# Optimization experiments

Measured on AMD Instinct MI355X. Metric: run time of the kernel, lower is better.

Reference implementation:

```python
import jax, jax.numpy as jnp
import numpy as np

# module hyperparameters (from init_kwargs)
STRIDE, PAD, DIL = 1, 1, 1
GROUPS, DG = 1, 1
KH, KW = 3, 3
CIN, COUT = 256, 256


def _mdcn_forward(x, offset, mask, weight, bias):
    B, C, H, W = x.shape
    Cout = weight.shape[0]
    K = KH * KW
    Ho = (H + 2 * PAD - (DIL * (KH - 1) + 1)) // STRIDE + 1
    Wo = (W + 2 * PAD - (DIL * (KW - 1) + 1)) // STRIDE + 1
    Cg = C // DG

    # offset channel layout: ((g*K + k)*2 + {0: dy, 1: dx})
    off = offset.reshape(B, DG, KH, KW, 2, Ho, Wo)
    base_y = (jnp.arange(Ho) * STRIDE - PAD)[None, :] + DIL * jnp.arange(KH)[:, None]  # [KH,Ho]
    base_x = (jnp.arange(Wo) * STRIDE - PAD)[None, :] + DIL * jnp.arange(KW)[:, None]  # [KW,Wo]
    sy = base_y[None, None, :, None, :, None].astype(x.dtype) + off[:, :, :, :, 0]  # [B,DG,KH,KW,Ho,Wo]
    sx = base_x[None, None, None, :, None, :].astype(x.dtype) + off[:, :, :, :, 1]

    y0f = jnp.floor(sy); x0f = jnp.floor(sx)
    wy = sy - y0f; wx = sx - x0f
    y0 = y0f.astype(jnp.int32); x0 = x0f.astype(jnp.int32)

    xg = x.reshape(B, DG, Cg, H * W)

    def corner(yc, xc, w):
        valid = (yc >= 0) & (yc < H) & (xc >= 0) & (xc < W)
        idx = jnp.clip(yc, 0, H - 1) * W + jnp.clip(xc, 0, W - 1)  # [B,DG,KH,KW,Ho,Wo]
        v = jnp.take_along_axis(xg, idx.reshape(B, DG, 1, -1), axis=3)  # [B,DG,Cg,K*Ho*Wo]
        v = v.reshape(B, DG, Cg, KH, KW, Ho, Wo)
        return v * (w * valid.astype(x.dtype))[:, :, None]

    val = (corner(y0, x0, (1 - wy) * (1 - wx))
           + corner(y0, x0 + 1, (1 - wy) * wx)
           + corner(y0 + 1, x0, wy * (1 - wx))
           + corner(y0 + 1, x0 + 1, wy * wx))  # [B,DG,Cg,KH,KW,Ho,Wo]

    cols = val * mask.reshape(B, DG, 1, KH, KW, Ho, Wo)
    cols = cols.reshape(B, GROUPS, (C // GROUPS) * K, Ho * Wo)
    wg = weight.reshape(GROUPS, Cout // GROUPS, (C // GROUPS) * K)
    out = jnp.einsum('gok,bgkp->bgop', wg, cols).reshape(B, Cout, Ho, Wo)
    return out + bias[None, :, None, None]


def setup_inputs() -> dict:
    key = jax.random.key(0)
    k1, k2, k3, k4 = jax.random.split(key, 4)
    B, H, W = 4, 64, 64
    x = jax.random.normal(k1, (B, CIN, H, W), dtype=jnp.float32)
    offset = jax.random.normal(k2, (B, 2 * DG * KH * KW, H, W), dtype=jnp.float32)
    mask = jax.random.uniform(k3, (B, DG * KH * KW, H, W), dtype=jnp.float32)
    stdv = 1.0 / np.sqrt(CIN * KH * KW)
    weight = jax.random.uniform(k4, (COUT, CIN // GROUPS, KH, KW), dtype=jnp.float32,
                                minval=-stdv, maxval=stdv)
    bias = jnp.zeros((COUT,), dtype=jnp.float32)
    return {"x": x, "offset": offset, "mask": mask, "weight": weight, "bias": bias}


def reference(x, offset, mask, weight, bias):
    return _mdcn_forward(x, offset, mask, weight, bias)
```

## Files before the change

### kernel.cpp

```cpp
#include <hip/hip_runtime.h>
#include <hip/hip_bf16.h>
#include <stdint.h>

#define KDIM 2304

typedef __bf16 bf16_t;
typedef bf16_t bf16x8 __attribute__((ext_vector_type(8)));
typedef float f32x4 __attribute__((ext_vector_type(4)));
typedef float f32x2 __attribute__((ext_vector_type(2)));

__device__ __forceinline__ float b2f_lo(uint32_t u) {
  union { uint32_t i; float f; } c; c.i = u << 16; return c.f;
}
__device__ __forceinline__ float b2f_hi(uint32_t u) {
  union { uint32_t i; float f; } c; c.i = u & 0xffff0000u; return c.f;
}
__device__ __forceinline__ uint32_t pk_bf16(float a, float b) {
  __hip_bfloat162 h = __float22bfloat162_rn(make_float2(a, b));
  union { __hip_bfloat162 h; uint32_t u; } c; c.h = h; return c.u;
}

__device__ __forceinline__ uint4 blend8(const uint4 d[4], const float cw[4]) {
  f32x2 f0 = {0.f, 0.f}, f1 = {0.f, 0.f}, f2 = {0.f, 0.f}, f3 = {0.f, 0.f};
#pragma unroll
  for (int c = 0; c < 4; ++c) {
    f32x2 wc = {cw[c], cw[c]};
    f0 += wc * f32x2{b2f_lo(d[c].x), b2f_hi(d[c].x)};
    f1 += wc * f32x2{b2f_lo(d[c].y), b2f_hi(d[c].y)};
    f2 += wc * f32x2{b2f_lo(d[c].z), b2f_hi(d[c].z)};
    f3 += wc * f32x2{b2f_lo(d[c].w), b2f_hi(d[c].w)};
  }
  uint4 o;
  o.x = pk_bf16(f0.x, f0.y);
  o.y = pk_bf16(f1.x, f1.y);
  o.z = pk_bf16(f2.x, f2.y);
  o.w = pk_bf16(f3.x, f3.y);
  return o;
}

__global__ __launch_bounds__(256) void k_prep(const float* __restrict__ x,
                                              uint16_t* __restrict__ xt,
                                              const float* __restrict__ w,
                                              uint16_t* __restrict__ wt2) {
  int tid = threadIdx.x;
  if (blockIdx.x < 1024) {
    __shared__ float tile[64][65];
    int b = blockIdx.x >> 8;
    int cgrp = (blockIdx.x >> 6) & 3;
    int sgrp = blockIdx.x & 63;
    int c0 = cgrp << 6, s0 = sgrp << 6;
#pragma unroll
    for (int it = 0; it < 4; ++it) {
      int f = tid + it * 256;
      int rr = f >> 4, col = (f & 15) << 2;
      float4 v = *(const float4*)&x[((size_t)(b * 256 + c0 + rr)) * 4096 + s0 + col];
      tile[rr][col + 0] = v.x;
      tile[rr][col + 1] = v.y;
      tile[rr][col + 2] = v.z;
      tile[rr][col + 3] = v.w;
    }
    __syncthreads();
    int sp = tid >> 2, cb = (tid & 3) * 16;
    uint4 o1, o2;
    o1.x = pk_bf16(tile[cb + 0][sp], tile[cb + 1][sp]);
    o1.y = pk_bf16(tile[cb + 2][sp], tile[cb + 3][sp]);
    o1.z = pk_bf16(tile[cb + 4][sp], tile[cb + 5][sp]);
    o1.w = pk_bf16(tile[cb + 6][sp], tile[cb + 7][sp]);
    o2.x = pk_bf16(tile[cb + 8][sp], tile[cb + 9][sp]);
    o2.y = pk_bf16(tile[cb + 10][sp], tile[cb + 11][sp]);
    o2.z = pk_bf16(tile[cb + 12][sp], tile[cb + 13][sp]);
    o2.w = pk_bf16(tile[cb + 14][sp], tile[cb + 15][sp]);
    uint16_t* dst = &xt[((size_t)(b * 4096 + s0 + sp)) * 256 + c0 + cb];
    *(uint4*)dst = o1;
    *(uint4*)(dst + 8) = o2;
  } else {
    __shared__ float wl[2304];
    int row = blockIdx.x - 1024;
    const float* wrow = w + (size_t)row * KDIM;
    for (int i2 = tid; i2 < 2304; i2 += 256) wl[i2] = wrow[i2];
    __syncthreads();
    int strip = row >> 4, r16 = row & 15;
    for (int c = tid; c < 288; c += 256) {
      int tap = c >> 5, rem = c & 31;
      int w64 = rem >> 3, kh = (rem >> 2) & 1, seg = rem & 3;
      int i = tap * 4 + w64;
      int cin0 = w64 * 64 + kh * 32 + seg * 8;
      int lanex = seg * 16 + r16;
      uint16_t* dst = wt2 + (size_t)i * 16384 + (size_t)(strip * 128 + kh * 64 + lanex) * 8;
      uint4 o;
      o.x = pk_bf16(wl[(cin0 + 0) * 9 + tap], wl[(cin0 + 1) * 9 + tap]);
      o.y = pk_bf16(wl[(cin0 + 2) * 9 + tap], wl[(cin0 + 3) * 9 + tap]);
      o.z = pk_bf16(wl[(cin0 + 4) * 9 + tap], wl[(cin0 + 5) * 9 + tap]);
      o.w = pk_bf16(wl[(cin0 + 6) * 9 + tap], wl[(cin0 + 7) * 9 + tap]);
      *(uint4*)dst = o;
    }
  }
}

__device__ __forceinline__ void mk_corners(int tap, int p, int ho,
                                           const float* s_off, const float* s_msk,
                                           float cw[4], int cpo[4]) {
  int kh = tap / 3, kw = tap - kh * 3;
  float dy = s_off[(2 * tap) * 64 + p];
  float dx = s_off[(2 * tap + 1) * 64 + p];
  float mm = s_msk[tap * 64 + p];
  float sy = (float)(ho - 1 + kh) + dy;
  float sx = (float)(p - 1 + kw) + dx;
  float fy = floorf(sy), fx = floorf(sx);
  int y0 = (int)fy, x0 = (int)fx;
  float wy = sy - fy, wx = sx - fx;
#pragma unroll
  for (int cy = 0; cy < 2; ++cy) {
#pragma unroll
    for (int cx = 0; cx < 2; ++cx) {
      int y = y0 + cy, xx = x0 + cx;
      float wgt = (cy ? wy : 1.f - wy) * (cx ? wx : 1.f - wx) * mm;
      bool v = ((unsigned)y < 64u) && ((unsigned)xx < 64u);
      wgt = v ? wgt : 0.f;
      int yc = min(max(y, 0), 63), xc = min(max(xx, 0), 63);
      cw[cy * 2 + cx] = wgt;
      cpo[cy * 2 + cx] = ((yc << 6) + xc) * 256;
    }
  }
}

__global__ __launch_bounds__(1024, 4) void k_fused(const uint16_t* __restrict__ xt,
                                                   const uint16_t* __restrict__ wt2,
                                                   const float* __restrict__ off,
                                                   const float* __restrict__ msk,
                                                   const float* __restrict__ bias,
                                                   float* __restrict__ out) {
  constexpr int ROWU = 272;
  constexpr int BUFU = 64 * ROWU;
  __shared__ __align__(16) uint16_t Bs[2 * BUFU];
  __shared__ float s_off[18 * 64];
  __shared__ float s_msk[9 * 64];

  int tid = threadIdx.x;
  int swz = ((int)blockIdx.x & 7) * 32 + ((int)blockIdx.x >> 3);
  int b = swz >> 6, ho = swz & 63;

  const float* offb = off + (size_t)b * 18 * 4096 + ho * 64;
  for (int i = tid; i < 18 * 64; i += 1024)
    s_off[i] = offb[(size_t)(i >> 6) * 4096 + (i & 63)];
  const float* mskb = msk + (size_t)b * 9 * 4096 + ho * 64;
  for (int i = tid; i < 9 * 64; i += 1024)
    s_msk[i] = mskb[(size_t)(i >> 6) * 4096 + (i & 63)];

  int lane = tid & 63, wv = tid >> 6;
  int wm = wv >> 1, wn = wv & 1;
  int q = lane >> 4, r = lane & 15;
  int p = tid >> 4, cg16 = tid & 15;
  int sA = cg16 >> 3, cg = cg16 & 7;
  const uint16_t* xtb = xt + (size_t)b * 1048576 + cg * 8;
  int chwA = sA * 64, chwB = chwA + 128;
  int ch = cg ^ (p & 7);
  int wcolA = p * ROWU + sA * 64 + ch * 8;
  int wcolB = wcolA + 128;

  f32x4 acc[2][2];
#pragma unroll
  for (int mi = 0; mi < 2; ++mi)
#pragma unroll
    for (int ni = 0; ni < 2; ++ni) acc[mi][ni] = f32x4{0.f, 0.f, 0.f, 0.f};

  __syncthreads();

  float cw[4];
  int cpo[4];
  uint4 dnvA[4], dnvB[4];

  int c0 = (q ^ (r & 7)) << 3;
  int c1 = c0 ^ 32;
  int rowb0 = (wn * 32 + r) * ROWU;

  mk_corners(0, p, ho, s_off, s_msk, cw, cpo);
#pragma unroll
  for (int c = 0; c < 4; ++c) dnvA[c] = *(const uint4*)(xtb + cpo[c] + chwA);
#pragma unroll
  for (int c = 0; c < 4; ++c) dnvB[c] = *(const uint4*)(xtb + cpo[c] + chwB);
  *(uint4*)(Bs + wcolA) = blend8(dnvA, cw);
  *(uint4*)(Bs + wcolB) = blend8(dnvB, cw);
  __syncthreads();

#define PHASE(S)                                                                \
    {                                                                           \
      const uint16_t* wp = wpb + (S) * 16384;                                   \
      bf16x8 a00 = *(const bf16x8*)(wp);                           \
      bf16x8 a01 = *(const bf16x8*)(wp + 512);                     \
      bf16x8 a10 = *(const bf16x8*)(wp + 1024);                    \
      bf16x8 a11 = *(const bf16x8*)(wp + 1536);                    \
      const uint16_t* br = bsrow + rowb0 + (S) * 64;                            \
      bf16x8 b0k0 = *(const bf16x8*)(br + c0);                                  \
      bf16x8 b0k1 = *(const bf16x8*)(br + c1);                                  \
      bf16x8 b1k0 = *(const bf16x8*)(br + 16 * ROWU + c0);                      \
      bf16x8 b1k1 = *(const bf16x8*)(br + 16 * ROWU + c1);                      \
      __builtin_amdgcn_s_setprio(1);                                            \
      acc[0][0] = __builtin_amdgcn_mfma_f32_16x16x32_bf16(a00, b0k0, acc[0][0], 0, 0, 0); \
      acc[0][1] = __builtin_amdgcn_mfma_f32_16x16x32_bf16(a00, b1k0, acc[0][1], 0, 0, 0); \
      acc[1][0] = __builtin_amdgcn_mfma_f32_16x16x32_bf16(a10, b0k0, acc[1][0], 0, 0, 0); \
      acc[1][1] = __builtin_amdgcn_mfma_f32_16x16x32_bf16(a10, b1k0, acc[1][1], 0, 0, 0); \
      acc[0][0] = __builtin_amdgcn_mfma_f32_16x16x32_bf16(a01, b0k1, acc[0][0], 0, 0, 0); \
      acc[0][1] = __builtin_amdgcn_mfma_f32_16x16x32_bf16(a01, b1k1, acc[0][1], 0, 0, 0); \
      acc[1][0] = __builtin_amdgcn_mfma_f32_16x16x32_bf16(a11, b0k1, acc[1][0], 0, 0, 0); \
      acc[1][1] = __builtin_amdgcn_mfma_f32_16x16x32_bf16(a11, b1k1, acc[1][1], 0, 0, 0); \
      __builtin_amdgcn_s_setprio(0);                                            \
    }

#pragma unroll 1
  for (int i = 0; i < 9; ++i) {
    if (i < 8) {
      mk_corners(i + 1, p, ho, s_off, s_msk, cw, cpo);
#pragma unroll
      for (int c = 0; c < 4; ++c) dnvA[c] = *(const uint4*)(xtb + cpo[c] + chwA);
#pragma unroll
      for (int c = 0; c < 4; ++c) dnvB[c] = *(const uint4*)(xtb + cpo[c] + chwB);
    }
    const uint16_t* wpb = wt2 + (size_t)(4 * i) * 16384 + wm * 2048 + lane * 8;
    const uint16_t* bsrow = Bs + (i & 1) * BUFU;
    PHASE(0)
    __builtin_amdgcn_sched_barrier(0);
    PHASE(1)
    __builtin_amdgcn_sched_barrier(0);
    PHASE(2)
    __builtin_amdgcn_sched_barrier(0);
    PHASE(3)
    if (i < 8) {
      uint16_t* wdst = Bs + ((i + 1) & 1) * BUFU;
      *(uint4*)(wdst + wcolA) = blend8(dnvA, cw);
      *(uint4*)(wdst + wcolB) = blend8(dnvB, cw);
    }
    __syncthreads();
  }
#undef PHASE

#pragma unroll
  for (int mi = 0; mi < 2; ++mi) {
#pragma unroll
    for (int j = 0; j < 4; ++j) {
      int m = wm * 32 + mi * 16 + q * 4 + j;
      float bv = bias[m];
#pragma unroll
      for (int ni = 0; ni < 2; ++ni) {
        int wog = wn * 32 + ni * 16 + r;
        out[((size_t)(b * 256 + m)) * 4096 + ho * 64 + wog] = acc[mi][ni][j] + bv;
      }
    }
  }
}

extern "C" void kernel_launch(void* const* d_in, const int* in_sizes, int n_in,
                              void* d_out, int out_size, void* d_ws, size_t ws_size,
                              hipStream_t stream) {
  (void)in_sizes; (void)n_in; (void)out_size; (void)ws_size;
  const float* x      = (const float*)d_in[0];
  const float* offset = (const float*)d_in[1];
  const float* mask   = (const float*)d_in[2];
  const float* weight = (const float*)d_in[3];
  const float* bias   = (const float*)d_in[4];
  float* out = (float*)d_out;

  uint8_t* ws = (uint8_t*)d_ws;
  uint16_t* xt  = (uint16_t*)ws;
  uint16_t* wt2 = (uint16_t*)(ws + 8388608);

  k_prep<<<dim3(1280), 256, 0, stream>>>(x, xt, weight, wt2);
  k_fused<<<dim3(256), 1024, 0, stream>>>(xt, wt2, offset, mask, bias, out);
}
```

Before: 119.0 us.

## Software-pipeline MFMA operand loads and interleave gather/blend across phases

Restructures the K-loop so the weight (A) and LDS (B) fragments for the next phase are loaded into a second register set while the current phase's MFMAs run. The offset-corner gathers and bilinear blends for the next tap are spread across the phases instead of being issued all at once up front. This hides global and LDS latency behind matrix math. The cost is more live vector registers, which may lower occupancy or cause spills.

```diff
diff --git a/kernel.cpp b/kernel.cpp
--- a/kernel.cpp
+++ b/kernel.cpp
@@ -169,70 +169,92 @@
   float cw[4];
   int cpo[4];
   uint4 dnvA[4], dnvB[4];
+  uint4 oA, oB;
+  bf16x8 X00, X01, X10, X11, Y00, Y01, Y10, Y11;
+  bf16x8 U0k0, U0k1, U1k0, U1k1, V0k0, V0k1, V1k0, V1k1;
 
   int c0 = (q ^ (r & 7)) << 3;
   int c1 = c0 ^ 32;
   int rowb0 = (wn * 32 + r) * ROWU;
 
+#define LOAD_A(P, BASE)                                                         \
+  P##00 = *(const bf16x8*)(BASE);                                               \
+  P##01 = *(const bf16x8*)((BASE) + 512);                                       \
+  P##10 = *(const bf16x8*)((BASE) + 1024);                                      \
+  P##11 = *(const bf16x8*)((BASE) + 1536);
+#define LOAD_B(P, OFS)                                                          \
+  P##0k0 = *(const bf16x8*)(bsrow + rowb0 + (OFS) + c0);                        \
+  P##0k1 = *(const bf16x8*)(bsrow + rowb0 + (OFS) + c1);                        \
+  P##1k0 = *(const bf16x8*)(bsrow + rowb0 + 16 * ROWU + (OFS) + c0);            \
+  P##1k1 = *(const bf16x8*)(bsrow + rowb0 + 16 * ROWU + (OFS) + c1);
+#define MFMA8(A, B)                                                             \
+  __builtin_amdgcn_s_setprio(1);                                                \
+  acc[0][0] = __builtin_amdgcn_mfma_f32_16x16x32_bf16(A##00, B##0k0, acc[0][0], 0, 0, 0); \
+  acc[0][1] = __builtin_amdgcn_mfma_f32_16x16x32_bf16(A##00, B##1k0, acc[0][1], 0, 0, 0); \
+  acc[1][0] = __builtin_amdgcn_mfma_f32_16x16x32_bf16(A##10, B##0k0, acc[1][0], 0, 0, 0); \
+  acc[1][1] = __builtin_amdgcn_mfma_f32_16x16x32_bf16(A##10, B##1k0, acc[1][1], 0, 0, 0); \
+  acc[0][0] = __builtin_amdgcn_mfma_f32_16x16x32_bf16(A##01, B##0k1, acc[0][0], 0, 0, 0); \
+  acc[0][1] = __builtin_amdgcn_mfma_f32_16x16x32_bf16(A##01, B##1k1, acc[0][1], 0, 0, 0); \
+  acc[1][0] = __builtin_amdgcn_mfma_f32_16x16x32_bf16(A##11, B##0k1, acc[1][0], 0, 0, 0); \
+  acc[1][1] = __builtin_amdgcn_mfma_f32_16x16x32_bf16(A##11, B##1k1, acc[1][1], 0, 0, 0); \
+  __builtin_amdgcn_s_setprio(0);
+
   mk_corners(0, p, ho, s_off, s_msk, cw, cpo);
 #pragma unroll
   for (int c = 0; c < 4; ++c) dnvA[c] = *(const uint4*)(xtb + cpo[c] + chwA);
 #pragma unroll
   for (int c = 0; c < 4; ++c) dnvB[c] = *(const uint4*)(xtb + cpo[c] + chwB);
+  {
+    const uint16_t* wp0 = wt2 + wm * 2048 + lane * 8;
+    LOAD_A(X, wp0)
+  }
   *(uint4*)(Bs + wcolA) = blend8(dnvA, cw);
   *(uint4*)(Bs + wcolB) = blend8(dnvB, cw);
   __syncthreads();
 
-#define PHASE(S)                                                                \
-    {                                                                           \
-      const uint16_t* wp = wpb + (S) * 16384;                                   \
-      bf16x8 a00 = *(const bf16x8*)(wp);                           \
-      bf16x8 a01 = *(const bf16x8*)(wp + 512);                     \
-      bf16x8 a10 = *(const bf16x8*)(wp + 1024);                    \
-      bf16x8 a11 = *(const bf16x8*)(wp + 1536);                    \
-      const uint16_t* br = bsrow + rowb0 + (S) * 64;                            \
-      bf16x8 b0k0 = *(const bf16x8*)(br + c0);                                  \
-      bf16x8 b0k1 = *(const bf16x8*)(br + c1);                                  \
-      bf16x8 b1k0 = *(const bf16x8*)(br + 16 * ROWU + c0);                      \
-      bf16x8 b1k1 = *(const bf16x8*)(br + 16 * ROWU + c1);                      \
-      __builtin_amdgcn_s_setprio(1);                                            \
-      acc[0][0] = __builtin_amdgcn_mfma_f32_16x16x32_bf16(a00, b0k0, acc[0][0], 0, 0, 0); \
-      acc[0][1] = __builtin_amdgcn_mfma_f32_16x16x32_bf16(a00, b1k0, acc[0][1], 0, 0, 0); \
-      acc[1][0] = __builtin_amdgcn_mfma_f32_16x16x32_bf16(a10, b0k0, acc[1][0], 0, 0, 0); \
-      acc[1][1] = __builtin_amdgcn_mfma_f32_16x16x32_bf16(a10, b1k0, acc[1][1], 0, 0, 0); \
-      acc[0][0] = __builtin_amdgcn_mfma_f32_16x16x32_bf16(a01, b0k1, acc[0][0], 0, 0, 0); \
-      acc[0][1] = __builtin_amdgcn_mfma_f32_16x16x32_bf16(a01, b1k1, acc[0][1], 0, 0, 0); \
-      acc[1][0] = __builtin_amdgcn_mfma_f32_16x16x32_bf16(a11, b0k1, acc[1][0], 0, 0, 0); \
-      acc[1][1] = __builtin_amdgcn_mfma_f32_16x16x32_bf16(a11, b1k1, acc[1][1], 0, 0, 0); \
-      __builtin_amdgcn_s_setprio(0);                                            \
-    }
-
 #pragma unroll 1
   for (int i = 0; i < 9; ++i) {
-    if (i < 8) {
-      mk_corners(i + 1, p, ho, s_off, s_msk, cw, cpo);
-#pragma unroll
-      for (int c = 0; c < 4; ++c) dnvA[c] = *(const uint4*)(xtb + cpo[c] + chwA);
-#pragma unroll
-      for (int c = 0; c < 4; ++c) dnvB[c] = *(const uint4*)(xtb + cpo[c] + chwB);
-    }
     const uint16_t* wpb = wt2 + (size_t)(4 * i) * 16384 + wm * 2048 + lane * 8;
     const uint16_t* bsrow = Bs + (i & 1) * BUFU;
-    PHASE(0)
+    bool more = (i < 8);
+    LOAD_B(U, 0)
+    if (more) {
+      mk_corners(i + 1, p, ho, s_off, s_msk, cw, cpo);
+#pragma unroll
+      for (int c = 0; c < 4; ++c) dnvA[c] = *(const uint4*)(xtb + cpo[c] + chwA);
+    }
+    LOAD_A(Y, wpb + 16384)
+    LOAD_B(V, 64)
+    MFMA8(X, U)
     __builtin_amdgcn_sched_barrier(0);
-    PHASE(1)
+    if (more) {
+#pragma unroll
+      for (int c = 0; c < 4; ++c) dnvB[c] = *(const uint4*)(xtb + cpo[c] + chwB);
+    }
+    LOAD_A(X, wpb + 2 * 16384)
+    LOAD_B(U, 2 * 64)
+    MFMA8(Y, V)
     __builtin_amdgcn_sched_barrier(0);
-    PHASE(2)
+    if (more) oA = blend8(dnvA, cw);
+    LOAD_A(Y, wpb + 3 * 16384)
+    LOAD_B(V, 3 * 64)
+    MFMA8(X, U)
     __builtin_amdgcn_sched_barrier(0);
-    PHASE(3)
-    if (i < 8) {
+    if (more) {
+      oB = blend8(dnvB, cw);
+      LOAD_A(X, wpb + 4 * 16384)
+    }
+    MFMA8(Y, V)
+    if (more) {
       uint16_t* wdst = Bs + ((i + 1) & 1) * BUFU;
-      *(uint4*)(wdst + wcolA) = blend8(dnvA, cw);
-      *(uint4*)(wdst + wcolB) = blend8(dnvB, cw);
+      *(uint4*)(wdst + wcolA) = oA;
+      *(uint4*)(wdst + wcolB) = oB;
     }
     __syncthreads();
   }
-#undef PHASE
+#undef LOAD_A
+#undef LOAD_B
+#undef MFMA8
 
 #pragma unroll
   for (int mi = 0; mi < 2; ++mi) {
```

Measured after the change: 203.1 us. 1.71x slower.
